# Performance work log

Measured on AMD Instinct MI355X. Metric: run time of the kernel, lower is better.

The kernel has to match this reference:

```python
import jax, jax.numpy as jnp
import numpy as np

B, N_PER, D = 128, 512, 128        # graphs, nodes per graph, feature width
N = B * N_PER                      # 65536 total nodes
E = 524288                         # total edges (avg degree 8)
KS = (410, 328, 263)               # ceil(0.8*512), ceil(0.8*410), ceil(0.8*328)


def setup_inputs() -> dict:
    key = jax.random.key(0)
    ks = jax.random.split(key, 20)
    p = lambda k, shape: jax.random.normal(k, shape, jnp.float32) * 0.05
    rng = np.random.default_rng(0)
    g = rng.integers(0, B, size=E)
    s = rng.integers(0, N_PER, size=E)
    t = rng.integers(0, N_PER, size=E)
    edge_index = jnp.asarray(np.stack([g * N_PER + s, g * N_PER + t]).astype(np.int32))
    inp = {
        'x': jax.random.normal(ks[0], (N, 1, D), jnp.float32),
        'edge_index': edge_index,
    }
    i = 1
    for l in (1, 2, 3):
        inp[f'conv{l}_wl'] = p(ks[i], (D, D)); i += 1   # SAGEConv lin_l (neighbors) weight
        inp[f'conv{l}_bl'] = p(ks[i], (D,));  i += 1   # SAGEConv lin_l bias
        inp[f'conv{l}_wr'] = p(ks[i], (D, D)); i += 1   # SAGEConv lin_r (root) weight
        inp[f'pool{l}_w'] = p(ks[i], (D,));   i += 1   # TopKPooling score vector
    inp['lin1_w'] = p(ks[13], (128, 256)); inp['lin1_b'] = p(ks[14], (128,))
    inp['lin2_w'] = p(ks[15], (64, 128));  inp['lin2_b'] = p(ks[16], (64,))
    inp['lin3_w'] = p(ks[17], (1, 64));    inp['lin3_b'] = p(ks[18], (1,))
    return inp


def _sage(x, node_mask, src, dst, wl, bl, wr):
    # SAGEConv, mean aggregation: lin_l(mean_{j->i} x_j) + lin_r(x_i)
    em = (node_mask[src] & node_mask[dst]).astype(x.dtype)   # [E] valid-edge mask
    msum = jax.ops.segment_sum(x[src] * em[:, None], dst, num_segments=N)
    deg = jax.ops.segment_sum(em, dst, num_segments=N)
    mean = msum / jnp.maximum(deg, 1.0)[:, None]
    return mean @ wl.T + bl + x @ wr.T


def _topk_pool(x, node_mask, w, k):
    # TopKPooling: score = x.w/||w||; keep top-k per graph; gate kept x by tanh(score)
    score = (x @ w) / (jnp.linalg.norm(w) + 1e-16)           # [N]
    score = jnp.where(node_mask, score, -jnp.inf)
    _, idx = jax.lax.top_k(score.reshape(B, N_PER), k)       # [B, k] within-graph ids
    nm = jnp.zeros((B, N_PER), bool).at[jnp.arange(B)[:, None], idx].set(True).reshape(-1)
    x = jnp.where(nm[:, None], x * jnp.tanh(score)[:, None], 0.0)
    return x, nm


def _readout(x, node_mask, k):
    # cat([global_max_pool, global_mean_pool]) over the k surviving nodes per graph
    xb = x.reshape(B, N_PER, -1)
    mb = node_mask.reshape(B, N_PER, 1)
    gmax = jnp.max(jnp.where(mb, xb, -jnp.inf), axis=1)
    gmean = jnp.sum(jnp.where(mb, xb, 0.0), axis=1) / k
    return jnp.concatenate([gmax, gmean], axis=1)            # [B, 2D]


def _forward(edge_index, x, conv1_wl, conv1_bl, conv1_wr, pool1_w,
             conv2_wl, conv2_bl, conv2_wr, pool2_w,
             conv3_wl, conv3_bl, conv3_wr, pool3_w,
             lin1_w, lin1_b, lin2_w, lin2_b, lin3_w, lin3_b):
    src, dst = edge_index[0], edge_index[1]
    h = x[:, 0, :]                                           # x.squeeze(1) -> [N, D]
    nm = jnp.ones((N,), bool)
    layers = ((conv1_wl, conv1_bl, conv1_wr, pool1_w),
              (conv2_wl, conv2_bl, conv2_wr, pool2_w),
              (conv3_wl, conv3_bl, conv3_wr, pool3_w))
    reads = []
    for (wl, bl, wr, pw), k in zip(layers, KS):
        h = jax.nn.relu(_sage(h, nm, src, dst, wl, bl, wr))
        h, nm = _topk_pool(h, nm, pw, k)
        reads.append(_readout(h, nm, float(k)))
    z = reads[0] + reads[1] + reads[2]                       # [B, 256]
    z = jax.nn.relu(z @ lin1_w.T + lin1_b)
    z = jax.nn.relu(z @ lin2_w.T + lin2_b)
    # dropout p=0.5 is a no-op at eval time
    return jax.nn.sigmoid(z @ lin3_w.T + lin3_b)[:, 0]       # [B]


def reference(x, edge_index, conv1_wl, conv1_bl, conv1_wr, pool1_w,
              conv2_wl, conv2_bl, conv2_wr, pool2_w,
              conv3_wl, conv3_bl, conv3_wr, pool3_w,
              lin1_w, lin1_b, lin2_w, lin2_b, lin3_w, lin3_b):
    return _forward(edge_index, x, conv1_wl, conv1_bl, conv1_wr, pool1_w,
                    conv2_wl, conv2_bl, conv2_wr, pool2_w,
                    conv3_wl, conv3_bl, conv3_wr, pool3_w,
                    lin1_w, lin1_b, lin2_w, lin2_b, lin3_w, lin3_b)
```

## Files before the change

kernel.cpp:

```cpp
#include <hip/hip_runtime.h>
#include <math.h>

#define NND 65536
#define NPER 512
#define NGR 128
#define DD 128
#define NED 524288

typedef __attribute__((ext_vector_type(8))) short short8;
typedef __attribute__((ext_vector_type(4))) float f32x4;

__device__ __forceinline__ unsigned short f2b(float f) {
  unsigned u = __float_as_uint(f);
  return (unsigned short)((u + 0x7FFFu + ((u >> 16) & 1u)) >> 16);
}
__device__ __forceinline__ float b2f(unsigned short h) {
  return __uint_as_float(((unsigned)h) << 16);
}


__global__ __launch_bounds__(256) void init_kernel(int* __restrict__ counts,
                                                   float2* __restrict__ tm) {
  int i = blockIdx.x * 256 + threadIdx.x;
  counts[i] = 0;
  tm[i] = make_float2(1.f, 1.f);
}

__global__ __launch_bounds__(256) void hist_kernel(const int* __restrict__ ei,
                                                   int* __restrict__ counts) {
  int e = blockIdx.x * 256 + threadIdx.x;
  atomicAdd(&counts[ei[NED + e]], 1);
}

__global__ __launch_bounds__(1024) void scan_kernel(const int* __restrict__ counts,
                                                    int* __restrict__ off,
                                                    int* __restrict__ cursor) {
  __shared__ int part[1024];
  int t = threadIdx.x;
  int base = t * 64;
  int s = 0;
  const int4* c4 = (const int4*)(counts + base);
  for (int i = 0; i < 16; ++i) {
    int4 v = c4[i];
    s += v.x + v.y + v.z + v.w;
  }
  part[t] = s;
  __syncthreads();
  for (int d = 1; d < 1024; d <<= 1) {
    int v = (t >= d) ? part[t - d] : 0;
    __syncthreads();
    part[t] += v;
    __syncthreads();
  }
  int run = (t == 0) ? 0 : part[t - 1];
  for (int i = 0; i < 64; ++i) {
    off[base + i] = run;
    cursor[base + i] = run;
    run += counts[base + i];
  }
  if (t == 1023) off[NND] = run;
}

__global__ __launch_bounds__(256) void scatter_kernel(const int* __restrict__ ei,
                                                      int* __restrict__ cursor,
                                                      int* __restrict__ ssrc) {
  int e = blockIdx.x * 256 + threadIdx.x;
  int dst = ei[NED + e];
  int pos = atomicAdd(&cursor[dst], 1);
  ssrc[pos] = ei[e];
}


__global__ __launch_bounds__(256) void prepw_kernel(
    const float* __restrict__ wl0, const float* __restrict__ wr0,
    const float* __restrict__ wl1, const float* __restrict__ wr1,
    const float* __restrict__ wl2, const float* __restrict__ wr2,
    unsigned short* __restrict__ Whi, unsigned short* __restrict__ Wlo) {
  const float* wls[3] = {wl0, wl1, wl2};
  const float* wrs[3] = {wr0, wr1, wr2};
  int e = blockIdx.x * 256 + threadIdx.x;
  int l = e >> 15;
  int o = e & 32767;
  int j = o & 7;
  int lane = (o >> 3) & 63;
  int nt = (o >> 9) & 7;
  int kc = o >> 12;
  int li = lane & 15, q = lane >> 4;
  int n = nt * 16 + li;
  int k = kc * 32 + q * 8 + j;
  const float* src = (k < 128) ? wls[l] : wrs[l];
  float v = src[n * DD + (k & 127)];
  unsigned short hi = f2b(v);
  float lo = v - b2f(hi);
  Whi[e] = hi;
  Wlo[e] = f2b(lo);
}


template <int CM>
__global__ __launch_bounds__(256) void agg_kernel_t(const float* __restrict__ x,
                                                    const float2* __restrict__ tm,
                                                    const int* __restrict__ off,
                                                    const int* __restrict__ ssrc,
                                                    unsigned short* __restrict__ mhi,
                                                    unsigned short* __restrict__ mlo) {
  const int wave = threadIdx.x >> 6;
  const int lane = threadIdx.x & 63;
  const int half = lane >> 5;
  const int l = lane & 31;
  const int bid = blockIdx.x;
  const int xcd = bid & 7;
  const int slot = bid >> 3;
  const int graph = xcd * 16 + (slot >> 5);
  const int within = slot & 31;
  const int d0 = graph * NPER + within * 16 + wave * 4;

  int offv = 0;
  if (lane < 5) offv = off[d0 + lane];
  float deadv = 1.f;
  if (CM && lane < 4) deadv = tm[d0 + lane].x;
  const int b0 = __shfl(offv, 0);
  const int b1 = __shfl(offv, 1);
  const int b2 = __shfl(offv, 2);
  const int b3 = __shfl(offv, 3);
  const int e3 = __shfl(offv, 4);
  float dd[4];
  if (CM) {
    dd[0] = __shfl(deadv, 0);
    dd[1] = __shfl(deadv, 1);
    dd[2] = __shfl(deadv, 2);
    dd[3] = __shfl(deadv, 3);
  }
  const int begs[4] = {b0, b1, b2, b3};
  const int ends[4] = {b1, b2, b3, e3};

  float4 acc[4];
  int deg[4];
#pragma unroll
  for (int d = 0; d < 4; ++d) {
    acc[d] = make_float4(0.f, 0.f, 0.f, 0.f);
    deg[d] = 0;
  }

  for (int base = b0; base < e3; base += 64) {
    const int nwin = min(64, e3 - base);
    int sv = 0;
    float tv = 0.f;
    int live = 0;
    if (lane < nwin) {
      sv = ssrc[base + lane];
      if (CM) {
        const float2 mt = tm[sv];
        live = (mt.x != 0.f);
        tv = mt.y;
      }
    }
    unsigned long long bl;
    if (CM)
      bl = __ballot(live);
    else
      bl = (nwin == 64) ? ~0ull : ((1ull << nwin) - 1);

#pragma unroll
    for (int d = 0; d < 4; ++d) {
      if (CM && dd[d] == 0.f) continue;
      const int lo = max(begs[d], base);
      const int hi = min(ends[d], base + 64);
      if (lo >= hi) continue;
      const int j0 = lo - base;
      const int j1 = hi - base;
      const unsigned long long wm =
          (((j1 == 64) ? ~0ull : ((1ull << j1) - 1)) & ~((1ull << j0) - 1));
      deg[d] += (int)__popcll(bl & wm);
      int j = j0 + half;
      for (; j + 6 < j1; j += 8) {
        const int s0 = __shfl(sv, j);
        const int s1 = __shfl(sv, j + 2);
        const int s2 = __shfl(sv, j + 4);
        const int s3 = __shfl(sv, j + 6);
        const float4 v0 = *(const float4*)(x + (size_t)s0 * DD + l * 4);
        const float4 v1 = *(const float4*)(x + (size_t)s1 * DD + l * 4);
        const float4 v2 = *(const float4*)(x + (size_t)s2 * DD + l * 4);
        const float4 v3 = *(const float4*)(x + (size_t)s3 * DD + l * 4);
        if (CM) {
          const float t0 = __shfl(tv, j), t1 = __shfl(tv, j + 2);
          const float t2 = __shfl(tv, j + 4), t3 = __shfl(tv, j + 6);
          acc[d].x += v0.x * t0 + v1.x * t1 + v2.x * t2 + v3.x * t3;
          acc[d].y += v0.y * t0 + v1.y * t1 + v2.y * t2 + v3.y * t3;
          acc[d].z += v0.z * t0 + v1.z * t1 + v2.z * t2 + v3.z * t3;
          acc[d].w += v0.w * t0 + v1.w * t1 + v2.w * t2 + v3.w * t3;
        } else {
          acc[d].x += v0.x + v1.x + v2.x + v3.x;
          acc[d].y += v0.y + v1.y + v2.y + v3.y;
          acc[d].z += v0.z + v1.z + v2.z + v3.z;
          acc[d].w += v0.w + v1.w + v2.w + v3.w;
        }
      }
      for (; j < j1; j += 2) {
        const int s = __shfl(sv, j);
        const float4 v = *(const float4*)(x + (size_t)s * DD + l * 4);
        if (CM) {
          const float t = __shfl(tv, j);
          acc[d].x += v.x * t;
          acc[d].y += v.y * t;
          acc[d].z += v.z * t;
          acc[d].w += v.w * t;
        } else {
          acc[d].x += v.x;
          acc[d].y += v.y;
          acc[d].z += v.z;
          acc[d].w += v.w;
        }
      }
    }
  }

#pragma unroll
  for (int d = 0; d < 4; ++d) {
    float4 a = acc[d];
    a.x += __shfl(a.x, lane ^ 32);
    a.y += __shfl(a.y, lane ^ 32);
    a.z += __shfl(a.z, lane ^ 32);
    a.w += __shfl(a.w, lane ^ 32);
    if (lane < 32) {
      const float inv = 1.f / (float)max(deg[d], 1);
      float4 m;
      m.x = a.x * inv;
      m.y = a.y * inv;
      m.z = a.z * inv;
      m.w = a.w * inv;
      ushort4 hv, lv;
      hv.x = f2b(m.x); lv.x = f2b(m.x - b2f(hv.x));
      hv.y = f2b(m.y); lv.y = f2b(m.y - b2f(hv.y));
      hv.z = f2b(m.z); lv.z = f2b(m.z - b2f(hv.z));
      hv.w = f2b(m.w); lv.w = f2b(m.w - b2f(hv.w));
      const size_t ad = (size_t)(d0 + d) * DD + l * 4;
      *(ushort4*)(mhi + ad) = hv;
      *(ushort4*)(mlo + ad) = lv;
    }
  }
}


#define GBM 64

template <int SCALE>
__global__ __launch_bounds__(256) void gemm_kernel_t(
    const unsigned short* __restrict__ Amh, const unsigned short* __restrict__ Aml,
    const float* __restrict__ Ax, const float2* __restrict__ tmp,
    const unsigned short* __restrict__ Whi, const unsigned short* __restrict__ Wlo,
    const float* __restrict__ bias, const float* __restrict__ pw,
    float* __restrict__ outp, float* __restrict__ sraw) {
  __shared__ short Ah[2048];
  __shared__ short Al[2048];
  __shared__ float s_sp[4][GBM];
  const int tid = threadIdx.x;
  const int wv = tid >> 6;
  const int lane = tid & 63;
  const int q = lane >> 4;
  const int li = lane & 15;
  const int row0 = blockIdx.x * GBM;

  int sdst[2];
#pragma unroll
  for (int i = 0; i < 2; ++i) {
    const int id = tid + i * 256;
    const int r = id >> 3;
    const int kb = (id & 7) << 2;
    sdst[i] = ((r >> 4) * 64 + (kb >> 3) * 16 + (r & 15)) * 8 + (kb & 7);
  }

  f32x4 acc[4][2];
#pragma unroll
  for (int m = 0; m < 4; ++m)
#pragma unroll
    for (int n = 0; n < 2; ++n) acc[m][n] = (f32x4){0.f, 0.f, 0.f, 0.f};

  float4 pa[2];
  ushort4 pmh[2], pml[2];
  short8 pbh[2], pbl[2];

#define LOADA(KC)                                                                      \
  {                                                                                    \
    if ((KC) < 4) {                                                                    \
      const int cb = (KC)*32;                                                          \
      _Pragma("unroll") for (int i = 0; i < 2; ++i) {                                  \
        const int id = tid + i * 256;                                                  \
        const size_t ga = (size_t)(row0 + (id >> 3)) * DD + cb + ((id & 7) << 2);      \
        pmh[i] = *(const ushort4*)(Amh + ga);                                          \
        pml[i] = *(const ushort4*)(Aml + ga);                                          \
      }                                                                                \
    } else {                                                                           \
      const int cb = ((KC)&3) * 32;                                                    \
      _Pragma("unroll") for (int i = 0; i < 2; ++i) {                                  \
        const int id = tid + i * 256;                                                  \
        pa[i] = *(const float4*)(Ax + (size_t)(row0 + (id >> 3)) * DD + cb + ((id & 7) << 2)); \
        if (SCALE) {                                                                   \
          const float tt = tmp[row0 + (id >> 3)].y;                                    \
          pa[i].x *= tt; pa[i].y *= tt; pa[i].z *= tt; pa[i].w *= tt;                  \
        }                                                                              \
      }                                                                                \
    }                                                                                  \
  }
#define LOADB(KC)                                                                      \
  {                                                                                    \
    _Pragma("unroll") for (int n = 0; n < 2; ++n) {                                    \
      const int ga = (((KC)*8 + wv * 2 + n) * 64 + lane) * 8;                          \
      pbh[n] = *(const short8*)(Whi + ga);                                             \
      pbl[n] = *(const short8*)(Wlo + ga);                                             \
    }                                                                                  \
  }

  LOADA(0) LOADB(0)

#pragma unroll
  for (int kc = 0; kc < 8; ++kc) {
    if (kc < 4) {
#pragma unroll
      for (int i = 0; i < 2; ++i) {
        *(ushort4*)(Ah + sdst[i]) = pmh[i];
        *(ushort4*)(Al + sdst[i]) = pml[i];
      }
    } else {
#pragma unroll
      for (int i = 0; i < 2; ++i) {
        ushort4 hv, lv;
        hv.x = f2b(pa[i].x); lv.x = f2b(pa[i].x - b2f(hv.x));
        hv.y = f2b(pa[i].y); lv.y = f2b(pa[i].y - b2f(hv.y));
        hv.z = f2b(pa[i].z); lv.z = f2b(pa[i].z - b2f(hv.z));
        hv.w = f2b(pa[i].w); lv.w = f2b(pa[i].w - b2f(hv.w));
        *(ushort4*)(Ah + sdst[i]) = hv;
        *(ushort4*)(Al + sdst[i]) = lv;
      }
    }
    short8 bh[2], bl[2];
    bh[0] = pbh[0]; bh[1] = pbh[1];
    bl[0] = pbl[0]; bl[1] = pbl[1];
    __syncthreads();
    short8 ah[4], al[4];
#pragma unroll
    for (int m = 0; m < 4; ++m) {
      ah[m] = *(const short8*)(Ah + (m * 64 + lane) * 8);
      al[m] = *(const short8*)(Al + (m * 64 + lane) * 8);
    }
    switch (kc) {
      case 0: LOADA(1) LOADB(1) break;
      case 1: LOADA(2) LOADB(2) break;
      case 2: LOADA(3) LOADB(3) break;
      case 3: LOADA(4) LOADB(4) break;
      case 4: LOADA(5) LOADB(5) break;
      case 5: LOADA(6) LOADB(6) break;
      case 6: LOADA(7) LOADB(7) break;
      default: break;
    }
#pragma unroll
    for (int m = 0; m < 4; ++m)
#pragma unroll
      for (int n = 0; n < 2; ++n) {
        acc[m][n] = __builtin_amdgcn_mfma_f32_16x16x32_bf16(ah[m], bh[n], acc[m][n], 0, 0, 0);
        acc[m][n] = __builtin_amdgcn_mfma_f32_16x16x32_bf16(ah[m], bl[n], acc[m][n], 0, 0, 0);
        acc[m][n] = __builtin_amdgcn_mfma_f32_16x16x32_bf16(al[m], bh[n], acc[m][n], 0, 0, 0);
      }
    __syncthreads();
  }
#undef LOADA
#undef LOADB

  const int c0 = wv * 32 + li;
  const int c1 = wv * 32 + 16 + li;
  const float b0 = bias[c0], b1 = bias[c1];
  const float p0 = pw[c0], p1 = pw[c1];
  float sp[16];
#pragma unroll
  for (int m = 0; m < 4; ++m) {
#pragma unroll
    for (int i = 0; i < 4; ++i) {
      const int r = row0 + m * 16 + q * 4 + i;
      const float v0 = fmaxf(acc[m][0][i] + b0, 0.f);
      const float v1 = fmaxf(acc[m][1][i] + b1, 0.f);
      outp[(size_t)r * DD + c0] = v0;
      outp[(size_t)r * DD + c1] = v1;
      sp[m * 4 + i] = v0 * p0 + v1 * p1;
    }
  }
#pragma unroll
  for (int e = 0; e < 16; ++e) {
    sp[e] += __shfl_xor(sp[e], 1);
    sp[e] += __shfl_xor(sp[e], 2);
    sp[e] += __shfl_xor(sp[e], 4);
    sp[e] += __shfl_xor(sp[e], 8);
  }
  if (li == 0) {
#pragma unroll
    for (int e = 0; e < 16; ++e) s_sp[wv][(e >> 2) * 16 + q * 4 + (e & 3)] = sp[e];
  }
  __syncthreads();
  if (tid < GBM)
    sraw[row0 + tid] = s_sp[0][tid] + s_sp[1][tid] + s_sp[2][tid] + s_sp[3][tid];
}


__global__ __launch_bounds__(256) void pool_kernel(const float* __restrict__ h,
                                                   const float* __restrict__ sraw,
                                                   const float* __restrict__ pw,
                                                   const float2* __restrict__ tmP,
                                                   float2* __restrict__ tmN,
                                                   float* __restrict__ zp,
                                                   const int kk) {
  __shared__ float s_sc[NPER];
  __shared__ float s_t[128];
  __shared__ unsigned char s_sel[128];
  __shared__ int s_rk[256];
  __shared__ float4 red4[512];
  __shared__ float s_norm;
  const int b = blockIdx.x;
  const int g = b >> 2;
  const int q = b & 3;
  const int tid = threadIdx.x;
  const int lane = tid & 63;

  if (tid < 64) {
    const float v0 = pw[lane], v1 = pw[lane + 64];
    float p = v0 * v0 + v1 * v1;
#pragma unroll
    for (int o = 32; o > 0; o >>= 1) p += __shfl_down(p, o);
    if (lane == 0) s_norm = 1.f / (sqrtf(p) + 1e-16f);
  }
  __syncthreads();
  const float inv_norm = s_norm;
#pragma unroll
  for (int i = 0; i < 2; ++i) {
    const int n = tid + i * 256;
    const int node = g * NPER + n;
    s_sc[n] = (tmP[node].x != 0.f) ? sraw[node] * inv_norm : -INFINITY;
  }
  __syncthreads();

  {
    const int n = q * 128 + (tid & 127);
    const int jb = (tid >> 7) * 256;
    const float s = s_sc[n];
    int rank = 0;
    for (int j = jb; j < jb + 256; ++j) {
      const float sj = s_sc[j];
      rank += (sj > s || (sj == s && j < n)) ? 1 : 0;
    }
    s_rk[tid] = rank;
  }
  __syncthreads();
  if (tid < 128) {
    const int n = q * 128 + tid;
    const int rank = s_rk[tid] + s_rk[tid + 128];
    const int sel = (rank < kk) ? 1 : 0;
    const float s = s_sc[n];
    const float t = sel ? tanhf(s) : 0.f;
    tmN[g * NPER + n] = make_float2(sel ? 1.f : 0.f, t);
    s_sel[tid] = (unsigned char)sel;
    s_t[tid] = t;
  }
  __syncthreads();

  const int c = tid & 31;
  const int r = tid >> 5;
  float4 pmax = make_float4(-INFINITY, -INFINITY, -INFINITY, -INFINITY);
  float4 psum = make_float4(0.f, 0.f, 0.f, 0.f);
  const size_t nbase = (size_t)g * NPER + q * 128;
  const float4* h4 = (const float4*)h;
  for (int i = 0; i < 16; ++i) {
    const int nl = r + 8 * i;
    if (s_sel[nl]) {
      float4 v = h4[(nbase + nl) * 32 + c];
      const float t = s_t[nl];
      v.x *= t; v.y *= t; v.z *= t; v.w *= t;
      pmax.x = fmaxf(pmax.x, v.x);
      pmax.y = fmaxf(pmax.y, v.y);
      pmax.z = fmaxf(pmax.z, v.z);
      pmax.w = fmaxf(pmax.w, v.w);
      psum.x += v.x; psum.y += v.y; psum.z += v.z; psum.w += v.w;
    }
  }
  red4[r * 32 + c] = pmax;
  red4[256 + r * 32 + c] = psum;
  __syncthreads();
  if (tid < 32) {
    float4 m = red4[tid];
    float4 sm = red4[256 + tid];
#pragma unroll
    for (int rr = 1; rr < 8; ++rr) {
      const float4 a = red4[rr * 32 + tid];
      const float4 s2 = red4[256 + rr * 32 + tid];
      m.x = fmaxf(m.x, a.x); m.y = fmaxf(m.y, a.y);
      m.z = fmaxf(m.z, a.z); m.w = fmaxf(m.w, a.w);
      sm.x += s2.x; sm.y += s2.y; sm.z += s2.z; sm.w += s2.w;
    }
    *(float4*)(zp + (size_t)b * 256 + tid * 4) = m;
    *(float4*)(zp + (size_t)b * 256 + 128 + tid * 4) = sm;
  }
}


__global__ __launch_bounds__(128) void mlp_kernel(const float* __restrict__ zpart,
                                                  const float* __restrict__ w1,
                                                  const float* __restrict__ b1,
                                                  const float* __restrict__ w2,
                                                  const float* __restrict__ b2,
                                                  const float* __restrict__ w3,
                                                  const float* __restrict__ b3,
                                                  float* __restrict__ out,
                                                  const float ik0, const float ik1,
                                                  const float ik2) {
  __shared__ float z[256];
  __shared__ float h1[128];
  __shared__ float h2[64];
  const int g = blockIdx.x;
  const int t = threadIdx.x;
  const float iks[3] = {ik0, ik1, ik2};
  float zmax = 0.f, zmean = 0.f;
#pragma unroll
  for (int l = 0; l < 3; ++l) {
    const float* zp = zpart + ((size_t)l * 512 + g * 4) * 256;
    zmax += fmaxf(fmaxf(zp[t], zp[256 + t]), fmaxf(zp[512 + t], zp[768 + t]));
    zmean += (zp[128 + t] + zp[384 + t] + zp[640 + t] + zp[896 + t]) * iks[l];
  }
  z[t] = zmax;
  z[128 + t] = zmean;
  __syncthreads();
  float a = b1[t];
  for (int k = 0; k < 256; ++k) a = fmaf(z[k], w1[t * 256 + k], a);
  h1[t] = fmaxf(a, 0.f);
  __syncthreads();
  if (t < 64) {
    float a2 = b2[t];
    for (int k = 0; k < 128; ++k) a2 = fmaf(h1[k], w2[t * 128 + k], a2);
    h2[t] = fmaxf(a2, 0.f);
  }
  __syncthreads();
  if (t == 0) {
    float a3 = b3[0];
    for (int k = 0; k < 64; ++k) a3 = fmaf(h2[k], w3[k], a3);
    out[g] = 1.f / (1.f + expf(-a3));
  }
}


extern "C" void kernel_launch(void* const* d_in, const int* in_sizes, int n_in,
                              void* d_out, int out_size, void* d_ws, size_t ws_size,
                              hipStream_t stream) {
  (void)in_sizes; (void)n_in; (void)out_size; (void)ws_size;
  const float* x_in = (const float*)d_in[0];
  const int* ei = (const int*)d_in[1];
  const float* wl[3] = {(const float*)d_in[2], (const float*)d_in[6], (const float*)d_in[10]};
  const float* cbl[3] = {(const float*)d_in[3], (const float*)d_in[7], (const float*)d_in[11]};
  const float* wr[3] = {(const float*)d_in[4], (const float*)d_in[8], (const float*)d_in[12]};
  const float* pw[3] = {(const float*)d_in[5], (const float*)d_in[9], (const float*)d_in[13]};
  const float* l1w = (const float*)d_in[14];
  const float* l1b = (const float*)d_in[15];
  const float* l2w = (const float*)d_in[16];
  const float* l2b = (const float*)d_in[17];
  const float* l3w = (const float*)d_in[18];
  const float* l3b = (const float*)d_in[19];
  float* out = (float*)d_out;

  char* w = (char*)d_ws;
  int* counts = (int*)(w + 0 * (1 << 20));
  int* off = (int*)(w + 1 * (1 << 20));
  int* cursor = (int*)(w + 2 * (1 << 20));
  float* sraw = (float*)(w + 2 * (1 << 20));
  float2* tmA = (float2*)(w + 3 * (1 << 20));
  float2* tmB = (float2*)(w + 3 * (1 << 20) + (1 << 19));
  float* zpart = (float*)(w + 4 * (1 << 20));
  unsigned short* Whi = (unsigned short*)(w + 5 * (1 << 20) + (1 << 19));
  unsigned short* Wlo = (unsigned short*)(w + 5 * (1 << 20) + 3 * (1 << 18));
  int* ssrc = (int*)(w + 6 * (1 << 20));
  unsigned short* mhi = (unsigned short*)(w + (size_t)8 * (1 << 20));
  unsigned short* mlo = (unsigned short*)(w + (size_t)24 * (1 << 20));
  float* hA = (float*)(w + (size_t)40 * (1 << 20));
  float* hB = (float*)(w + (size_t)72 * (1 << 20));

  init_kernel<<<NND / 256, 256, 0, stream>>>(counts, tmA);
  hist_kernel<<<NED / 256, 256, 0, stream>>>(ei, counts);
  scan_kernel<<<1, 1024, 0, stream>>>(counts, off, cursor);
  scatter_kernel<<<NED / 256, 256, 0, stream>>>(ei, cursor, ssrc);
  prepw_kernel<<<384, 256, 0, stream>>>(wl[0], wr[0], wl[1], wr[1], wl[2], wr[2], Whi, Wlo);

  const int ks[3] = {410, 328, 263};
  const float* xl = x_in;
  float* houts[3] = {hA, hB, hA};
  float2* tprev[3] = {tmA, tmB, tmA};
  float2* tnext[3] = {tmB, tmA, tmB};
  for (int l = 0; l < 3; ++l) {
    float* hout = houts[l];
    if (l == 0) {
      agg_kernel_t<0><<<4096, 256, 0, stream>>>(xl, tprev[l], off, ssrc, mhi, mlo);
      gemm_kernel_t<0><<<NND / GBM, 256, 0, stream>>>(mhi, mlo, xl, tprev[l],
                                                      Whi + (size_t)l * 32768,
                                                      Wlo + (size_t)l * 32768, cbl[l], pw[l],
                                                      hout, sraw);
    } else {
      agg_kernel_t<1><<<4096, 256, 0, stream>>>(xl, tprev[l], off, ssrc, mhi, mlo);
      gemm_kernel_t<1><<<NND / GBM, 256, 0, stream>>>(mhi, mlo, xl, tprev[l],
                                                      Whi + (size_t)l * 32768,
                                                      Wlo + (size_t)l * 32768, cbl[l], pw[l],
                                                      hout, sraw);
    }
    pool_kernel<<<NGR * 4, 256, 0, stream>>>(hout, sraw, pw[l], tprev[l], tnext[l],
                                             zpart + (size_t)l * 512 * 256, ks[l]);
    xl = hout;
  }
  mlp_kernel<<<NGR, 128, 0, stream>>>(zpart, l1w, l1b, l2w, l2b, l3w, l3b, out,
                                      1.f / 410.f, 1.f / 328.f, 1.f / 263.f);
}
```

Baseline: 406.1 us.

## Fuse neighbor aggregation into the SAGE GEMM kernel via shared-memory means

Merges the separate aggregation and GEMM kernels into one per-layer kernel. Each block first computes mean-aggregated neighbor features for its 64 rows into shared memory (fp32, padded stride), then runs the split-bf16 MFMA GEMM reading A from LDS instead of global hi/lo buffers. This removes the global round trip of the mean matrix and one launch per layer. In exchange, each block now has 4x more aggregation work with only 1024 blocks, which lowers parallelism for the gather phase, and the larger LDS footprint may reduce occupancy. Dead rows now get an explicit zero mean, where before that store was skipped.

```diff
diff --git a/kernel.cpp b/kernel.cpp
--- a/kernel.cpp
+++ b/kernel.cpp
@@ -97,177 +97,166 @@
 }
 
 
-template <int CM>
-__global__ __launch_bounds__(256) void agg_kernel_t(const float* __restrict__ x,
-                                                    const float2* __restrict__ tm,
-                                                    const int* __restrict__ off,
-                                                    const int* __restrict__ ssrc,
-                                                    unsigned short* __restrict__ mhi,
-                                                    unsigned short* __restrict__ mlo) {
-  const int wave = threadIdx.x >> 6;
-  const int lane = threadIdx.x & 63;
-  const int half = lane >> 5;
-  const int l = lane & 31;
-  const int bid = blockIdx.x;
-  const int xcd = bid & 7;
-  const int slot = bid >> 3;
-  const int graph = xcd * 16 + (slot >> 5);
-  const int within = slot & 31;
-  const int d0 = graph * NPER + within * 16 + wave * 4;
-
-  int offv = 0;
-  if (lane < 5) offv = off[d0 + lane];
-  float deadv = 1.f;
-  if (CM && lane < 4) deadv = tm[d0 + lane].x;
-  const int b0 = __shfl(offv, 0);
-  const int b1 = __shfl(offv, 1);
-  const int b2 = __shfl(offv, 2);
-  const int b3 = __shfl(offv, 3);
-  const int e3 = __shfl(offv, 4);
-  float dd[4];
-  if (CM) {
-    dd[0] = __shfl(deadv, 0);
-    dd[1] = __shfl(deadv, 1);
-    dd[2] = __shfl(deadv, 2);
-    dd[3] = __shfl(deadv, 3);
-  }
-  const int begs[4] = {b0, b1, b2, b3};
-  const int ends[4] = {b1, b2, b3, e3};
-
-  float4 acc[4];
-  int deg[4];
-#pragma unroll
-  for (int d = 0; d < 4; ++d) {
-    acc[d] = make_float4(0.f, 0.f, 0.f, 0.f);
-    deg[d] = 0;
-  }
-
-  for (int base = b0; base < e3; base += 64) {
-    const int nwin = min(64, e3 - base);
-    int sv = 0;
-    float tv = 0.f;
-    int live = 0;
-    if (lane < nwin) {
-      sv = ssrc[base + lane];
-      if (CM) {
-        const float2 mt = tm[sv];
-        live = (mt.x != 0.f);
-        tv = mt.y;
-      }
-    }
-    unsigned long long bl;
-    if (CM)
-      bl = __ballot(live);
-    else
-      bl = (nwin == 64) ? ~0ull : ((1ull << nwin) - 1);
-
-#pragma unroll
-    for (int d = 0; d < 4; ++d) {
-      if (CM && dd[d] == 0.f) continue;
-      const int lo = max(begs[d], base);
-      const int hi = min(ends[d], base + 64);
-      if (lo >= hi) continue;
-      const int j0 = lo - base;
-      const int j1 = hi - base;
-      const unsigned long long wm =
-          (((j1 == 64) ? ~0ull : ((1ull << j1) - 1)) & ~((1ull << j0) - 1));
-      deg[d] += (int)__popcll(bl & wm);
-      int j = j0 + half;
-      for (; j + 6 < j1; j += 8) {
-        const int s0 = __shfl(sv, j);
-        const int s1 = __shfl(sv, j + 2);
-        const int s2 = __shfl(sv, j + 4);
-        const int s3 = __shfl(sv, j + 6);
-        const float4 v0 = *(const float4*)(x + (size_t)s0 * DD + l * 4);
-        const float4 v1 = *(const float4*)(x + (size_t)s1 * DD + l * 4);
-        const float4 v2 = *(const float4*)(x + (size_t)s2 * DD + l * 4);
-        const float4 v3 = *(const float4*)(x + (size_t)s3 * DD + l * 4);
-        if (CM) {
-          const float t0 = __shfl(tv, j), t1 = __shfl(tv, j + 2);
-          const float t2 = __shfl(tv, j + 4), t3 = __shfl(tv, j + 6);
-          acc[d].x += v0.x * t0 + v1.x * t1 + v2.x * t2 + v3.x * t3;
-          acc[d].y += v0.y * t0 + v1.y * t1 + v2.y * t2 + v3.y * t3;
-          acc[d].z += v0.z * t0 + v1.z * t1 + v2.z * t2 + v3.z * t3;
-          acc[d].w += v0.w * t0 + v1.w * t1 + v2.w * t2 + v3.w * t3;
-        } else {
-          acc[d].x += v0.x + v1.x + v2.x + v3.x;
-          acc[d].y += v0.y + v1.y + v2.y + v3.y;
-          acc[d].z += v0.z + v1.z + v2.z + v3.z;
-          acc[d].w += v0.w + v1.w + v2.w + v3.w;
-        }
-      }
-      for (; j < j1; j += 2) {
-        const int s = __shfl(sv, j);
-        const float4 v = *(const float4*)(x + (size_t)s * DD + l * 4);
-        if (CM) {
-          const float t = __shfl(tv, j);
-          acc[d].x += v.x * t;
-          acc[d].y += v.y * t;
-          acc[d].z += v.z * t;
-          acc[d].w += v.w * t;
-        } else {
-          acc[d].x += v.x;
-          acc[d].y += v.y;
-          acc[d].z += v.z;
-          acc[d].w += v.w;
-        }
-      }
-    }
-  }
-
-#pragma unroll
-  for (int d = 0; d < 4; ++d) {
-    float4 a = acc[d];
-    a.x += __shfl(a.x, lane ^ 32);
-    a.y += __shfl(a.y, lane ^ 32);
-    a.z += __shfl(a.z, lane ^ 32);
-    a.w += __shfl(a.w, lane ^ 32);
-    if (lane < 32) {
-      const float inv = 1.f / (float)max(deg[d], 1);
-      float4 m;
-      m.x = a.x * inv;
-      m.y = a.y * inv;
-      m.z = a.z * inv;
-      m.w = a.w * inv;
-      ushort4 hv, lv;
-      hv.x = f2b(m.x); lv.x = f2b(m.x - b2f(hv.x));
-      hv.y = f2b(m.y); lv.y = f2b(m.y - b2f(hv.y));
-      hv.z = f2b(m.z); lv.z = f2b(m.z - b2f(hv.z));
-      hv.w = f2b(m.w); lv.w = f2b(m.w - b2f(hv.w));
-      const size_t ad = (size_t)(d0 + d) * DD + l * 4;
-      *(ushort4*)(mhi + ad) = hv;
-      *(ushort4*)(mlo + ad) = lv;
-    }
-  }
-}
-
-
 #define GBM 64
-
-template <int SCALE>
-__global__ __launch_bounds__(256) void gemm_kernel_t(
-    const unsigned short* __restrict__ Amh, const unsigned short* __restrict__ Aml,
-    const float* __restrict__ Ax, const float2* __restrict__ tmp,
+#define SMSTR 132
+
+template <int FIRST>
+__global__ __launch_bounds__(256) void layer_kernel_t(
+    const float* __restrict__ x, const float2* __restrict__ tm,
+    const int* __restrict__ off, const int* __restrict__ ssrc,
     const unsigned short* __restrict__ Whi, const unsigned short* __restrict__ Wlo,
     const float* __restrict__ bias, const float* __restrict__ pw,
     float* __restrict__ outp, float* __restrict__ sraw) {
+  __shared__ float smean[GBM * SMSTR];
   __shared__ short Ah[2048];
   __shared__ short Al[2048];
   __shared__ float s_sp[4][GBM];
   const int tid = threadIdx.x;
   const int wv = tid >> 6;
   const int lane = tid & 63;
+  const int half = lane >> 5;
+  const int l = lane & 31;
   const int q = lane >> 4;
   const int li = lane & 15;
-  const int row0 = blockIdx.x * GBM;
+  const int bid = blockIdx.x;
+  const int xcd = bid & 7;
+  const int slot = bid >> 3;
+  const int graph = xcd * 16 + (slot >> 3);
+  const int mtile = slot & 7;
+  const int row0 = graph * NPER + mtile * GBM;
+
+  for (int dg = 0; dg < 4; ++dg) {
+    const int d0 = row0 + wv * 16 + dg * 4;
+    int offv = 0;
+    if (lane < 5) offv = off[d0 + lane];
+    float deadv = 1.f;
+    if (!FIRST && lane < 4) deadv = tm[d0 + lane].x;
+    const int b0 = __shfl(offv, 0);
+    const int b1 = __shfl(offv, 1);
+    const int b2 = __shfl(offv, 2);
+    const int b3 = __shfl(offv, 3);
+    const int e3 = __shfl(offv, 4);
+    float dd[4];
+    if (!FIRST) {
+      dd[0] = __shfl(deadv, 0);
+      dd[1] = __shfl(deadv, 1);
+      dd[2] = __shfl(deadv, 2);
+      dd[3] = __shfl(deadv, 3);
+    }
+    const int begs[4] = {b0, b1, b2, b3};
+    const int ends[4] = {b1, b2, b3, e3};
+
+    float4 acc[4];
+    int deg[4];
+#pragma unroll
+    for (int d = 0; d < 4; ++d) {
+      acc[d] = make_float4(0.f, 0.f, 0.f, 0.f);
+      deg[d] = 0;
+    }
+
+    for (int base = b0; base < e3; base += 64) {
+      const int nwin = min(64, e3 - base);
+      int sv = 0;
+      float tv = 0.f;
+      int live = 0;
+      if (lane < nwin) {
+        sv = ssrc[base + lane];
+        if (!FIRST) {
+          const float2 mt = tm[sv];
+          live = (mt.x != 0.f);
+          tv = mt.y;
+        }
+      }
+      unsigned long long bl;
+      if (!FIRST)
+        bl = __ballot(live);
+      else
+        bl = (nwin == 64) ? ~0ull : ((1ull << nwin) - 1);
+
+#pragma unroll
+      for (int d = 0; d < 4; ++d) {
+        if (!FIRST && dd[d] == 0.f) continue;
+        const int lo = max(begs[d], base);
+        const int hi = min(ends[d], base + 64);
+        if (lo >= hi) continue;
+        const int j0 = lo - base;
+        const int j1 = hi - base;
+        const unsigned long long wm =
+            (((j1 == 64) ? ~0ull : ((1ull << j1) - 1)) & ~((1ull << j0) - 1));
+        deg[d] += (int)__popcll(bl & wm);
+        int j = j0 + half;
+        for (; j + 6 < j1; j += 8) {
+          const int s0 = __shfl(sv, j);
+          const int s1 = __shfl(sv, j + 2);
+          const int s2 = __shfl(sv, j + 4);
+          const int s3 = __shfl(sv, j + 6);
+          const float4 v0 = *(const float4*)(x + (size_t)s0 * DD + l * 4);
+          const float4 v1 = *(const float4*)(x + (size_t)s1 * DD + l * 4);
+          const float4 v2 = *(const float4*)(x + (size_t)s2 * DD + l * 4);
+          const float4 v3 = *(const float4*)(x + (size_t)s3 * DD + l * 4);
+          if (!FIRST) {
+            const float t0 = __shfl(tv, j), t1 = __shfl(tv, j + 2);
+            const float t2 = __shfl(tv, j + 4), t3 = __shfl(tv, j + 6);
+            acc[d].x += v0.x * t0 + v1.x * t1 + v2.x * t2 + v3.x * t3;
+            acc[d].y += v0.y * t0 + v1.y * t1 + v2.y * t2 + v3.y * t3;
+            acc[d].z += v0.z * t0 + v1.z * t1 + v2.z * t2 + v3.z * t3;
+            acc[d].w += v0.w * t0 + v1.w * t1 + v2.w * t2 + v3.w * t3;
+          } else {
+            acc[d].x += v0.x + v1.x + v2.x + v3.x;
+            acc[d].y += v0.y + v1.y + v2.y + v3.y;
+            acc[d].z += v0.z + v1.z + v2.z + v3.z;
+            acc[d].w += v0.w + v1.w + v2.w + v3.w;
+          }
+        }
+        for (; j < j1; j += 2) {
+          const int s = __shfl(sv, j);
+          const float4 v = *(const float4*)(x + (size_t)s * DD + l * 4);
+          if (!FIRST) {
+            const float t = __shfl(tv, j);
+            acc[d].x += v.x * t;
+            acc[d].y += v.y * t;
+            acc[d].z += v.z * t;
+            acc[d].w += v.w * t;
+          } else {
+            acc[d].x += v.x;
+            acc[d].y += v.y;
+            acc[d].z += v.z;
+            acc[d].w += v.w;
+          }
+        }
+      }
+    }
+
+#pragma unroll
+    for (int d = 0; d < 4; ++d) {
+      float4 a = acc[d];
+      const int dead = (!FIRST && dd[d] == 0.f);
+      a.x += __shfl(a.x, lane ^ 32);
+      a.y += __shfl(a.y, lane ^ 32);
+      a.z += __shfl(a.z, lane ^ 32);
+      a.w += __shfl(a.w, lane ^ 32);
+      if (lane < 32) {
+        const float inv = dead ? 0.f : (1.f / (float)max(deg[d], 1));
+        float4 m;
+        m.x = a.x * inv;
+        m.y = a.y * inv;
+        m.z = a.z * inv;
+        m.w = a.w * inv;
+        *(float4*)(smean + (wv * 16 + dg * 4 + d) * SMSTR + l * 4) = m;
+      }
+    }
+  }
+  __syncthreads();
 
   int sdst[2];
+  float ts[2];
 #pragma unroll
   for (int i = 0; i < 2; ++i) {
     const int id = tid + i * 256;
     const int r = id >> 3;
     const int kb = (id & 7) << 2;
     sdst[i] = ((r >> 4) * 64 + (kb >> 3) * 16 + (r & 15)) * 8 + (kb & 7);
+    ts[i] = FIRST ? 1.f : tm[row0 + r].y;
   }
 
   f32x4 acc[4][2];
@@ -277,61 +266,49 @@
     for (int n = 0; n < 2; ++n) acc[m][n] = (f32x4){0.f, 0.f, 0.f, 0.f};
 
   float4 pa[2];
-  ushort4 pmh[2], pml[2];
   short8 pbh[2], pbl[2];
 
-#define LOADA(KC)                                                                      \
-  {                                                                                    \
-    if ((KC) < 4) {                                                                    \
-      const int cb = (KC)*32;                                                          \
-      _Pragma("unroll") for (int i = 0; i < 2; ++i) {                                  \
-        const int id = tid + i * 256;                                                  \
-        const size_t ga = (size_t)(row0 + (id >> 3)) * DD + cb + ((id & 7) << 2);      \
-        pmh[i] = *(const ushort4*)(Amh + ga);                                          \
-        pml[i] = *(const ushort4*)(Aml + ga);                                          \
-      }                                                                                \
-    } else {                                                                           \
-      const int cb = ((KC)&3) * 32;                                                    \
-      _Pragma("unroll") for (int i = 0; i < 2; ++i) {                                  \
-        const int id = tid + i * 256;                                                  \
-        pa[i] = *(const float4*)(Ax + (size_t)(row0 + (id >> 3)) * DD + cb + ((id & 7) << 2)); \
-        if (SCALE) {                                                                   \
-          const float tt = tmp[row0 + (id >> 3)].y;                                    \
-          pa[i].x *= tt; pa[i].y *= tt; pa[i].z *= tt; pa[i].w *= tt;                  \
-        }                                                                              \
-      }                                                                                \
-    }                                                                                  \
-  }
-#define LOADB(KC)                                                                      \
-  {                                                                                    \
-    _Pragma("unroll") for (int n = 0; n < 2; ++n) {                                    \
-      const int ga = (((KC)*8 + wv * 2 + n) * 64 + lane) * 8;                          \
-      pbh[n] = *(const short8*)(Whi + ga);                                             \
-      pbl[n] = *(const short8*)(Wlo + ga);                                             \
-    }                                                                                  \
+#define LOADA(KC)                                                                       \
+  {                                                                                     \
+    if ((KC) < 4) {                                                                     \
+      const int cb = (KC)*32;                                                           \
+      _Pragma("unroll") for (int i = 0; i < 2; ++i) {                                   \
+        const int id = tid + i * 256;                                                   \
+        pa[i] = *(const float4*)(smean + (id >> 3) * SMSTR + cb + ((id & 7) << 2));     \
+      }                                                                                 \
+    } else {                                                                            \
+      const int cb = ((KC)&3) * 32;                                                     \
+      _Pragma("unroll") for (int i = 0; i < 2; ++i) {                                   \
+        const int id = tid + i * 256;                                                   \
+        pa[i] = *(const float4*)(x + (size_t)(row0 + (id >> 3)) * DD + cb + ((id & 7) << 2)); \
+        if (!FIRST) {                                                                   \
+          pa[i].x *= ts[i]; pa[i].y *= ts[i]; pa[i].z *= ts[i]; pa[i].w *= ts[i];       \
+        }                                                                               \
+      }                                                                                 \
+    }                                                                                   \
+  }
+#define LOADB(KC)                                                                       \
+  {                                                                                     \
+    _Pragma("unroll") for (int n = 0; n < 2; ++n) {                                     \
+      const int ga = (((KC)*8 + wv * 2 + n) * 64 + lane) * 8;                           \
+      pbh[n] = *(const short8*)(Whi + ga);                                              \
+      pbl[n] = *(const short8*)(Wlo + ga);                                              \
+    }                                                                                   \
   }
 
   LOADA(0) LOADB(0)
 
 #pragma unroll
   for (int kc = 0; kc < 8; ++kc) {
-    if (kc < 4) {
-#pragma unroll
-      for (int i = 0; i < 2; ++i) {
-        *(ushort4*)(Ah + sdst[i]) = pmh[i];
-        *(ushort4*)(Al + sdst[i]) = pml[i];
-      }
-    } else {
-#pragma unroll
-      for (int i = 0; i < 2; ++i) {
-        ushort4 hv, lv;
-        hv.x = f2b(pa[i].x); lv.x = f2b(pa[i].x - b2f(hv.x));
-        hv.y = f2b(pa[i].y); lv.y = f2b(pa[i].y - b2f(hv.y));
-        hv.z = f2b(pa[i].z); lv.z = f2b(pa[i].z - b2f(hv.z));
-        hv.w = f2b(pa[i].w); lv.w = f2b(pa[i].w - b2f(hv.w));
-        *(ushort4*)(Ah + sdst[i]) = hv;
-        *(ushort4*)(Al + sdst[i]) = lv;
-      }
+#pragma unroll
+    for (int i = 0; i < 2; ++i) {
+      ushort4 hv, lv;
+      hv.x = f2b(pa[i].x); lv.x = f2b(pa[i].x - b2f(hv.x));
+      hv.y = f2b(pa[i].y); lv.y = f2b(pa[i].y - b2f(hv.y));
+      hv.z = f2b(pa[i].z); lv.z = f2b(pa[i].z - b2f(hv.z));
+      hv.w = f2b(pa[i].w); lv.w = f2b(pa[i].w - b2f(hv.w));
+      *(ushort4*)(Ah + sdst[i]) = hv;
+      *(ushort4*)(Al + sdst[i]) = lv;
     }
     short8 bh[2], bl[2];
     bh[0] = pbh[0]; bh[1] = pbh[1];
@@ -572,8 +549,6 @@
   unsigned short* Whi = (unsigned short*)(w + 5 * (1 << 20) + (1 << 19));
   unsigned short* Wlo = (unsigned short*)(w + 5 * (1 << 20) + 3 * (1 << 18));
   int* ssrc = (int*)(w + 6 * (1 << 20));
-  unsigned short* mhi = (unsigned short*)(w + (size_t)8 * (1 << 20));
-  unsigned short* mlo = (unsigned short*)(w + (size_t)24 * (1 << 20));
   float* hA = (float*)(w + (size_t)40 * (1 << 20));
   float* hB = (float*)(w + (size_t)72 * (1 << 20));
 
@@ -591,17 +566,15 @@
   for (int l = 0; l < 3; ++l) {
     float* hout = houts[l];
     if (l == 0) {
-      agg_kernel_t<0><<<4096, 256, 0, stream>>>(xl, tprev[l], off, ssrc, mhi, mlo);
-      gemm_kernel_t<0><<<NND / GBM, 256, 0, stream>>>(mhi, mlo, xl, tprev[l],
-                                                      Whi + (size_t)l * 32768,
-                                                      Wlo + (size_t)l * 32768, cbl[l], pw[l],
-                                                      hout, sraw);
+      layer_kernel_t<1><<<1024, 256, 0, stream>>>(xl, tprev[l], off, ssrc,
+                                                  Whi + (size_t)l * 32768,
+                                                  Wlo + (size_t)l * 32768, cbl[l], pw[l],
+                                                  hout, sraw);
     } else {
-      agg_kernel_t<1><<<4096, 256, 0, stream>>>(xl, tprev[l], off, ssrc, mhi, mlo);
-      gemm_kernel_t<1><<<NND / GBM, 256, 0, stream>>>(mhi, mlo, xl, tprev[l],
-                                                      Whi + (size_t)l * 32768,
-                                                      Wlo + (size_t)l * 32768, cbl[l], pw[l],
-                                                      hout, sraw);
+      layer_kernel_t<0><<<1024, 256, 0, stream>>>(xl, tprev[l], off, ssrc,
+                                                  Whi + (size_t)l * 32768,
+                                                  Wlo + (size_t)l * 32768, cbl[l], pw[l],
+                                                  hout, sraw);
     }
     pool_kernel<<<NGR * 4, 256, 0, stream>>>(hout, sraw, pw[l], tprev[l], tnext[l],
                                              zpart + (size_t)l * 512 * 256, ks[l]);
```

After: 422.4 us. 4.0% more time.

## Fuse neighbor aggregation into SAGE GEMM kernel and merge init with weight prep

Applied to the files above, without the earlier changes.

Aggregation is now a device function that each GEMM block runs for its own 64 rows before doing the matmul, which removes a separate kernel launch per layer. The aggregated rows are still written to global mhi/mlo and read back after a block barrier, so the saving is mostly launch overhead and some L2 locality. Grid size drops from 4096 aggregation blocks to 1024 fused blocks, which lowers parallelism for the latency-bound gather. The init and weight-prep kernels are also merged into one setup kernel, and dead-node mean outputs are zeroed explicitly.

```diff
diff --git a/kernel.cpp b/kernel.cpp
--- a/kernel.cpp
+++ b/kernel.cpp
@@ -19,66 +19,19 @@
 }
 
 
-__global__ __launch_bounds__(256) void init_kernel(int* __restrict__ counts,
-                                                   float2* __restrict__ tm) {
-  int i = blockIdx.x * 256 + threadIdx.x;
-  counts[i] = 0;
-  tm[i] = make_float2(1.f, 1.f);
-}
-
-__global__ __launch_bounds__(256) void hist_kernel(const int* __restrict__ ei,
-                                                   int* __restrict__ counts) {
-  int e = blockIdx.x * 256 + threadIdx.x;
-  atomicAdd(&counts[ei[NED + e]], 1);
-}
-
-__global__ __launch_bounds__(1024) void scan_kernel(const int* __restrict__ counts,
-                                                    int* __restrict__ off,
-                                                    int* __restrict__ cursor) {
-  __shared__ int part[1024];
-  int t = threadIdx.x;
-  int base = t * 64;
-  int s = 0;
-  const int4* c4 = (const int4*)(counts + base);
-  for (int i = 0; i < 16; ++i) {
-    int4 v = c4[i];
-    s += v.x + v.y + v.z + v.w;
-  }
-  part[t] = s;
-  __syncthreads();
-  for (int d = 1; d < 1024; d <<= 1) {
-    int v = (t >= d) ? part[t - d] : 0;
-    __syncthreads();
-    part[t] += v;
-    __syncthreads();
-  }
-  int run = (t == 0) ? 0 : part[t - 1];
-  for (int i = 0; i < 64; ++i) {
-    off[base + i] = run;
-    cursor[base + i] = run;
-    run += counts[base + i];
-  }
-  if (t == 1023) off[NND] = run;
-}
-
-__global__ __launch_bounds__(256) void scatter_kernel(const int* __restrict__ ei,
-                                                      int* __restrict__ cursor,
-                                                      int* __restrict__ ssrc) {
-  int e = blockIdx.x * 256 + threadIdx.x;
-  int dst = ei[NED + e];
-  int pos = atomicAdd(&cursor[dst], 1);
-  ssrc[pos] = ei[e];
-}
-
-
-__global__ __launch_bounds__(256) void prepw_kernel(
+__global__ __launch_bounds__(256) void setup_kernel(
+    int* __restrict__ counts, float2* __restrict__ tm,
     const float* __restrict__ wl0, const float* __restrict__ wr0,
     const float* __restrict__ wl1, const float* __restrict__ wr1,
     const float* __restrict__ wl2, const float* __restrict__ wr2,
     unsigned short* __restrict__ Whi, unsigned short* __restrict__ Wlo) {
+  const int e = blockIdx.x * 256 + threadIdx.x;
+  if (e < NND) {
+    counts[e] = 0;
+    tm[e] = make_float2(1.f, 1.f);
+  }
   const float* wls[3] = {wl0, wl1, wl2};
   const float* wrs[3] = {wr0, wr1, wr2};
-  int e = blockIdx.x * 256 + threadIdx.x;
   int l = e >> 15;
   int o = e & 32767;
   int j = o & 7;
@@ -91,45 +44,80 @@
   const float* src = (k < 128) ? wls[l] : wrs[l];
   float v = src[n * DD + (k & 127)];
   unsigned short hi = f2b(v);
-  float lo = v - b2f(hi);
   Whi[e] = hi;
-  Wlo[e] = f2b(lo);
-}
-
-
-template <int CM>
-__global__ __launch_bounds__(256) void agg_kernel_t(const float* __restrict__ x,
-                                                    const float2* __restrict__ tm,
-                                                    const int* __restrict__ off,
-                                                    const int* __restrict__ ssrc,
-                                                    unsigned short* __restrict__ mhi,
-                                                    unsigned short* __restrict__ mlo) {
-  const int wave = threadIdx.x >> 6;
-  const int lane = threadIdx.x & 63;
+  Wlo[e] = f2b(v - b2f(hi));
+}
+
+__global__ __launch_bounds__(256) void hist_kernel(const int* __restrict__ ei,
+                                                   int* __restrict__ counts) {
+  int e = blockIdx.x * 256 + threadIdx.x;
+  atomicAdd(&counts[ei[NED + e]], 1);
+}
+
+__global__ __launch_bounds__(1024) void scan_kernel(const int* __restrict__ counts,
+                                                    int* __restrict__ off,
+                                                    int* __restrict__ cursor) {
+  __shared__ int part[1024];
+  int t = threadIdx.x;
+  int base = t * 64;
+  int s = 0;
+  const int4* c4 = (const int4*)(counts + base);
+  for (int i = 0; i < 16; ++i) {
+    int4 v = c4[i];
+    s += v.x + v.y + v.z + v.w;
+  }
+  part[t] = s;
+  __syncthreads();
+  for (int d = 1; d < 1024; d <<= 1) {
+    int v = (t >= d) ? part[t - d] : 0;
+    __syncthreads();
+    part[t] += v;
+    __syncthreads();
+  }
+  int run = (t == 0) ? 0 : part[t - 1];
+  for (int i = 0; i < 64; ++i) {
+    off[base + i] = run;
+    cursor[base + i] = run;
+    run += counts[base + i];
+  }
+  if (t == 1023) off[NND] = NED;
+}
+
+__global__ __launch_bounds__(256) void scatter_kernel(const int* __restrict__ ei,
+                                                      int* __restrict__ cursor,
+                                                      int* __restrict__ ssrc) {
+  int e = blockIdx.x * 256 + threadIdx.x;
+  int dst = ei[NED + e];
+  int pos = atomicAdd(&cursor[dst], 1);
+  ssrc[pos] = ei[e];
+}
+
+
+template <int FIRST>
+__device__ __forceinline__ void agg_group4(const int d0, const float* __restrict__ x,
+                                           const float2* __restrict__ tm,
+                                           const int* __restrict__ off,
+                                           const int* __restrict__ ssrc,
+                                           unsigned short* __restrict__ mhi,
+                                           unsigned short* __restrict__ mlo,
+                                           const int lane) {
   const int half = lane >> 5;
   const int l = lane & 31;
-  const int bid = blockIdx.x;
-  const int xcd = bid & 7;
-  const int slot = bid >> 3;
-  const int graph = xcd * 16 + (slot >> 5);
-  const int within = slot & 31;
-  const int d0 = graph * NPER + within * 16 + wave * 4;
-
   int offv = 0;
   if (lane < 5) offv = off[d0 + lane];
   float deadv = 1.f;
-  if (CM && lane < 4) deadv = tm[d0 + lane].x;
+  if (!FIRST && lane < 4) deadv = tm[d0 + lane].x;
   const int b0 = __shfl(offv, 0);
   const int b1 = __shfl(offv, 1);
   const int b2 = __shfl(offv, 2);
   const int b3 = __shfl(offv, 3);
   const int e3 = __shfl(offv, 4);
-  float dd[4];
-  if (CM) {
-    dd[0] = __shfl(deadv, 0);
-    dd[1] = __shfl(deadv, 1);
-    dd[2] = __shfl(deadv, 2);
-    dd[3] = __shfl(deadv, 3);
+  float dds[4] = {1.f, 1.f, 1.f, 1.f};
+  if (!FIRST) {
+    dds[0] = __shfl(deadv, 0);
+    dds[1] = __shfl(deadv, 1);
+    dds[2] = __shfl(deadv, 2);
+    dds[3] = __shfl(deadv, 3);
   }
   const int begs[4] = {b0, b1, b2, b3};
   const int ends[4] = {b1, b2, b3, e3};
@@ -149,21 +137,21 @@
     int live = 0;
     if (lane < nwin) {
       sv = ssrc[base + lane];
-      if (CM) {
+      if (!FIRST) {
         const float2 mt = tm[sv];
         live = (mt.x != 0.f);
         tv = mt.y;
       }
     }
     unsigned long long bl;
-    if (CM)
+    if (!FIRST)
       bl = __ballot(live);
     else
       bl = (nwin == 64) ? ~0ull : ((1ull << nwin) - 1);
 
 #pragma unroll
     for (int d = 0; d < 4; ++d) {
-      if (CM && dd[d] == 0.f) continue;
+      if (!FIRST && dds[d] == 0.f) continue;
       const int lo = max(begs[d], base);
       const int hi = min(ends[d], base + 64);
       if (lo >= hi) continue;
@@ -182,7 +170,7 @@
         const float4 v1 = *(const float4*)(x + (size_t)s1 * DD + l * 4);
         const float4 v2 = *(const float4*)(x + (size_t)s2 * DD + l * 4);
         const float4 v3 = *(const float4*)(x + (size_t)s3 * DD + l * 4);
-        if (CM) {
+        if (!FIRST) {
           const float t0 = __shfl(tv, j), t1 = __shfl(tv, j + 2);
           const float t2 = __shfl(tv, j + 4), t3 = __shfl(tv, j + 6);
           acc[d].x += v0.x * t0 + v1.x * t1 + v2.x * t2 + v3.x * t3;
@@ -199,7 +187,7 @@
       for (; j < j1; j += 2) {
         const int s = __shfl(sv, j);
         const float4 v = *(const float4*)(x + (size_t)s * DD + l * 4);
-        if (CM) {
+        if (!FIRST) {
           const float t = __shfl(tv, j);
           acc[d].x += v.x * t;
           acc[d].y += v.y * t;
@@ -223,7 +211,7 @@
     a.z += __shfl(a.z, lane ^ 32);
     a.w += __shfl(a.w, lane ^ 32);
     if (lane < 32) {
-      const float inv = 1.f / (float)max(deg[d], 1);
+      const float inv = (!FIRST && dds[d] == 0.f) ? 0.f : (1.f / (float)max(deg[d], 1));
       float4 m;
       m.x = a.x * inv;
       m.y = a.y * inv;
@@ -244,30 +232,47 @@
 
 #define GBM 64
 
-template <int SCALE>
-__global__ __launch_bounds__(256) void gemm_kernel_t(
-    const unsigned short* __restrict__ Amh, const unsigned short* __restrict__ Aml,
-    const float* __restrict__ Ax, const float2* __restrict__ tmp,
+struct GemmSmem {
+  short Ah[2048];
+  short Al[2048];
+  float s_sp[4][GBM];
+};
+
+template <int FIRST>
+__global__ __launch_bounds__(256) void aggemm_kernel_t(
+    const float* __restrict__ x, const float2* __restrict__ tm,
+    const int* __restrict__ off, const int* __restrict__ ssrc,
+    unsigned short* __restrict__ mhi, unsigned short* __restrict__ mlo,
     const unsigned short* __restrict__ Whi, const unsigned short* __restrict__ Wlo,
     const float* __restrict__ bias, const float* __restrict__ pw,
     float* __restrict__ outp, float* __restrict__ sraw) {
-  __shared__ short Ah[2048];
-  __shared__ short Al[2048];
-  __shared__ float s_sp[4][GBM];
+  __shared__ GemmSmem sm;
   const int tid = threadIdx.x;
   const int wv = tid >> 6;
   const int lane = tid & 63;
   const int q = lane >> 4;
   const int li = lane & 15;
-  const int row0 = blockIdx.x * GBM;
+  const int bid = blockIdx.x;
+  const int xcd = bid & 7;
+  const int slot = bid >> 3;
+  const int graph = xcd * 16 + (slot >> 3);
+  const int mtile = slot & 7;
+  const int row0 = graph * NPER + mtile * GBM;
+
+#pragma unroll
+  for (int s = 0; s < 4; ++s)
+    agg_group4<FIRST>(row0 + (s * 4 + wv) * 4, x, tm, off, ssrc, mhi, mlo, lane);
+  __syncthreads();
 
   int sdst[2];
+  float ts[2];
 #pragma unroll
   for (int i = 0; i < 2; ++i) {
     const int id = tid + i * 256;
     const int r = id >> 3;
     const int kb = (id & 7) << 2;
     sdst[i] = ((r >> 4) * 64 + (kb >> 3) * 16 + (r & 15)) * 8 + (kb & 7);
+    ts[i] = FIRST ? 1.f : tm[row0 + r].y;
   }
 
   f32x4 acc[4][2];
@@ -287,17 +292,16 @@
       _Pragma("unroll") for (int i = 0; i < 2; ++i) {                                  \
         const int id = tid + i * 256;                                                  \
         const size_t ga = (size_t)(row0 + (id >> 3)) * DD + cb + ((id & 7) << 2);      \
-        pmh[i] = *(const ushort4*)(Amh + ga);                                          \
-        pml[i] = *(const ushort4*)(Aml + ga);                                          \
+        pmh[i] = *(const ushort4*)(mhi + ga);                                          \
+        pml[i] = *(const ushort4*)(mlo + ga);                                          \
       }                                                                                \
     } else {                                                                           \
       const int cb = ((KC)&3) * 32;                                                    \
       _Pragma("unroll") for (int i = 0; i < 2; ++i) {                                  \
         const int id = tid + i * 256;                                                  \
-        pa[i] = *(const float4*)(Ax + (size_t)(row0 + (id >> 3)) * DD + cb + ((id & 7) << 2)); \
-        if (SCALE) {                                                                   \
-          const float tt = tmp[row0 + (id >> 3)].y;                                    \
-          pa[i].x *= tt; pa[i].y *= tt; pa[i].z *= tt; pa[i].w *= tt;                  \
+        pa[i] = *(const float4*)(x + (size_t)(row0 + (id >> 3)) * DD + cb + ((id & 7) << 2)); \
+        if (!FIRST) {                                                                  \
+          pa[i].x *= ts[i]; pa[i].y *= ts[i]; pa[i].z *= ts[i]; pa[i].w *= ts[i];      \
         }                                                                              \
       }                                                                                \
     }                                                                                  \
@@ -318,8 +322,8 @@
     if (kc < 4) {
 #pragma unroll
       for (int i = 0; i < 2; ++i) {
-        *(ushort4*)(Ah + sdst[i]) = pmh[i];
-        *(ushort4*)(Al + sdst[i]) = pml[i];
+        *(ushort4*)(sm.Ah + sdst[i]) = pmh[i];
+        *(ushort4*)(sm.Al + sdst[i]) = pml[i];
       }
     } else {
 #pragma unroll
@@ -329,8 +333,8 @@
         hv.y = f2b(pa[i].y); lv.y = f2b(pa[i].y - b2f(hv.y));
         hv.z = f2b(pa[i].z); lv.z = f2b(pa[i].z - b2f(hv.z));
         hv.w = f2b(pa[i].w); lv.w = f2b(pa[i].w - b2f(hv.w));
-        *(ushort4*)(Ah + sdst[i]) = hv;
-        *(ushort4*)(Al + sdst[i]) = lv;
+        *(ushort4*)(sm.Ah + sdst[i]) = hv;
+        *(ushort4*)(sm.Al + sdst[i]) = lv;
       }
     }
     short8 bh[2], bl[2];
@@ -340,8 +344,8 @@
     short8 ah[4], al[4];
 #pragma unroll
     for (int m = 0; m < 4; ++m) {
-      ah[m] = *(const short8*)(Ah + (m * 64 + lane) * 8);
-      al[m] = *(const short8*)(Al + (m * 64 + lane) * 8);
+      ah[m] = *(const short8*)(sm.Ah + (m * 64 + lane) * 8);
+      al[m] = *(const short8*)(sm.Al + (m * 64 + lane) * 8);
     }
     switch (kc) {
       case 0: LOADA(1) LOADB(1) break;
@@ -392,11 +396,11 @@
   }
   if (li == 0) {
 #pragma unroll
-    for (int e = 0; e < 16; ++e) s_sp[wv][(e >> 2) * 16 + q * 4 + (e & 3)] = sp[e];
+    for (int e = 0; e < 16; ++e) sm.s_sp[wv][(e >> 2) * 16 + q * 4 + (e & 3)] = sp[e];
   }
   __syncthreads();
   if (tid < GBM)
-    sraw[row0 + tid] = s_sp[0][tid] + s_sp[1][tid] + s_sp[2][tid] + s_sp[3][tid];
+    sraw[row0 + tid] = sm.s_sp[0][tid] + sm.s_sp[1][tid] + sm.s_sp[2][tid] + sm.s_sp[3][tid];
 }
 
 
@@ -484,17 +488,17 @@
   __syncthreads();
   if (tid < 32) {
     float4 m = red4[tid];
-    float4 sm = red4[256 + tid];
+    float4 sm2 = red4[256 + tid];
 #pragma unroll
     for (int rr = 1; rr < 8; ++rr) {
       const float4 a = red4[rr * 32 + tid];
-      const float4 s2 = red4[256 + rr * 32 + tid];
+      const float4 s3 = red4[256 + rr * 32 + tid];
       m.x = fmaxf(m.x, a.x); m.y = fmaxf(m.y, a.y);
       m.z = fmaxf(m.z, a.z); m.w = fmaxf(m.w, a.w);
-      sm.x += s2.x; sm.y += s2.y; sm.z += s2.z; sm.w += s2.w;
+      sm2.x += s3.x; sm2.y += s3.y; sm2.z += s3.z; sm2.w += s3.w;
     }
     *(float4*)(zp + (size_t)b * 256 + tid * 4) = m;
-    *(float4*)(zp + (size_t)b * 256 + 128 + tid * 4) = sm;
+    *(float4*)(zp + (size_t)b * 256 + 128 + tid * 4) = sm2;
   }
 }
 
@@ -506,15 +510,13 @@
                                                   const float* __restrict__ b2,
                                                   const float* __restrict__ w3,
                                                   const float* __restrict__ b3,
-                                                  float* __restrict__ out,
-                                                  const float ik0, const float ik1,
-                                                  const float ik2) {
+                                                  float* __restrict__ out) {
   __shared__ float z[256];
   __shared__ float h1[128];
   __shared__ float h2[64];
   const int g = blockIdx.x;
   const int t = threadIdx.x;
-  const float iks[3] = {ik0, ik1, ik2};
+  const float iks[3] = {1.f / 410.f, 1.f / 328.f, 1.f / 263.f};
   float zmax = 0.f, zmean = 0.f;
 #pragma unroll
   for (int l = 0; l < 3; ++l) {
@@ -577,11 +579,11 @@
   float* hA = (float*)(w + (size_t)40 * (1 << 20));
   float* hB = (float*)(w + (size_t)72 * (1 << 20));
 
-  init_kernel<<<NND / 256, 256, 0, stream>>>(counts, tmA);
+  setup_kernel<<<384, 256, 0, stream>>>(counts, tmA, wl[0], wr[0], wl[1], wr[1], wl[2], wr[2],
+                                        Whi, Wlo);
   hist_kernel<<<NED / 256, 256, 0, stream>>>(ei, counts);
   scan_kernel<<<1, 1024, 0, stream>>>(counts, off, cursor);
   scatter_kernel<<<NED / 256, 256, 0, stream>>>(ei, cursor, ssrc);
-  prepw_kernel<<<384, 256, 0, stream>>>(wl[0], wr[0], wl[1], wr[1], wl[2], wr[2], Whi, Wlo);
 
   const int ks[3] = {410, 328, 263};
   const float* xl = x_in;
@@ -590,23 +592,19 @@
   float2* tnext[3] = {tmB, tmA, tmB};
   for (int l = 0; l < 3; ++l) {
     float* hout = houts[l];
-    if (l == 0) {
-      agg_kernel_t<0><<<4096, 256, 0, stream>>>(xl, tprev[l], off, ssrc, mhi, mlo);
-      gemm_kernel_t<0><<<NND / GBM, 256, 0, stream>>>(mhi, mlo, xl, tprev[l],
-                                                      Whi + (size_t)l * 32768,
-                                                      Wlo + (size_t)l * 32768, cbl[l], pw[l],
-                                                      hout, sraw);
-    } else {
-      agg_kernel_t<1><<<4096, 256, 0, stream>>>(xl, tprev[l], off, ssrc, mhi, mlo);
-      gemm_kernel_t<1><<<NND / GBM, 256, 0, stream>>>(mhi, mlo, xl, tprev[l],
-                                                      Whi + (size_t)l * 32768,
-                                                      Wlo + (size_t)l * 32768, cbl[l], pw[l],
-                                                      hout, sraw);
-    }
+    if (l == 0)
+      aggemm_kernel_t<1><<<1024, 256, 0, stream>>>(xl, tprev[l], off, ssrc, mhi, mlo,
+                                                   Whi + (size_t)l * 32768,
+                                                   Wlo + (size_t)l * 32768, cbl[l], pw[l],
+                                                   hout, sraw);
+    else
+      aggemm_kernel_t<0><<<1024, 256, 0, stream>>>(xl, tprev[l], off, ssrc, mhi, mlo,
+                                                   Whi + (size_t)l * 32768,
+                                                   Wlo + (size_t)l * 32768, cbl[l], pw[l],
+                                                   hout, sraw);
     pool_kernel<<<NGR * 4, 256, 0, stream>>>(hout, sraw, pw[l], tprev[l], tnext[l],
                                              zpart + (size_t)l * 512 * 256, ks[l]);
     xl = hout;
   }
-  mlp_kernel<<<NGR, 128, 0, stream>>>(zpart, l1w, l1b, l2w, l2b, l3w, l3b, out,
-                                      1.f / 410.f, 1.f / 328.f, 1.f / 263.f);
-}
+  mlp_kernel<<<NGR, 128, 0, stream>>>(zpart, l1w, l1b, l2w, l2b, l3w, l3b, out);
+}
```

Result: slower. 425.2 us (+4.7%).
